# Kernel tuning notes

Measured on AMD Instinct MI355X. Metric: run time of the kernel, lower is better.

## Reference

```python
import jax, jax.numpy as jnp
import numpy as np

SPARSITY = 0.5  # cur_sparsity set during training; 0.0 default would make masking a no-op
WEIGHT_BETA = 1.0
MASK_ALPHA1 = 1.0
MASK_ALPHA2 = 1.0


def binarize(mask_scores, sparsity):
    # SparseBinarizer.forward: prune (set to 0) the `num_prune` smallest scores globally.
    num_prune = int(mask_scores.size * sparsity)  # static: sparsity is a Python float
    flat = mask_scores.reshape(-1)
    prune_idx = jnp.argsort(flat)[:num_prune]
    mask = jnp.ones_like(flat).at[prune_idx].set(0.0)
    return mask.reshape(mask_scores.shape)


def setup_inputs() -> dict:
    key = jax.random.key(0)
    ks = jax.random.split(key, 9)
    out_f, in_f, r = 4096, 4096, 8
    tokens = 8192  # batch 4 * seq 2048
    return {
        "x": jax.random.normal(ks[0], (tokens, in_f), dtype=jnp.float32),
        "weight": jax.random.normal(ks[1], (out_f, in_f), dtype=jnp.float32) * 0.02,
        "bias": jax.random.normal(ks[2], (out_f,), dtype=jnp.float32) * 0.02,
        "weight_U": jax.random.normal(ks[3], (out_f, r), dtype=jnp.float32),
        "weight_V": jnp.zeros((r, in_f), dtype=jnp.float32),
        "mask_scores_A": jax.random.normal(ks[4], (out_f, r), dtype=jnp.float32),
        "mask_scores_B": jnp.zeros((r, in_f), dtype=jnp.float32),
        "mask_scores_R": jnp.zeros((out_f,), dtype=jnp.float32),
        "mask_scores_C": jnp.zeros((in_f,), dtype=jnp.float32),
    }


def reference(x, weight, bias, weight_U, weight_V, mask_scores_A, mask_scores_B,
              mask_scores_R, mask_scores_C):
    # weight = W + beta * U @ V   (low-rank weight reconstruction)
    w = weight + WEIGHT_BETA * (weight_U @ weight_V)
    # mask_scores = |w| + a1 * A @ B + a2 * (R[:,None] + C[None,:])
    mask_scores = (jnp.abs(w)
                   + MASK_ALPHA1 * (mask_scores_A @ mask_scores_B)
                   + MASK_ALPHA2 * (mask_scores_R[:, None] + mask_scores_C[None, :]))
    mask = binarize(mask_scores, SPARSITY)
    masked_weight = mask * w  # [out_f, in_f]
    # nn.Linear: x @ W^T + b
    return x @ masked_weight.T + bias
```

## Files before the change

kernel.cpp:

```cpp
#include <hip/hip_runtime.h>
#include <stdint.h>

#define TOKENS 8192
#define OUT_F  4096
#define IN_F   4096
#define RNK    8
#define RPB    4
#define KPRUNE 8388608u
#define CAP3   16384u

typedef unsigned short u16;
typedef float  f32x4  __attribute__((ext_vector_type(4)));
typedef short  bf16x8 __attribute__((ext_vector_type(8)));
typedef unsigned short u16x8 __attribute__((ext_vector_type(8)));

#define XB_OFF    0ull
#define WB_OFF    67108864ull
#define KEYS_OFF  100663296ull
#define CTL_OFF   167772160ull
#define H1_OFF    0
#define H2_OFF    16384
#define SEL_OFF   32768
#define CNT3_OFF  32800
#define LIST3_OFF 32804
#define CTL_ZERO_U32 8201

__device__ __forceinline__ u16 f2bf(float f) {
    uint32_t u = __float_as_uint(f);
    u += 0x7fffu + ((u >> 16) & 1u);
    return (u16)(u >> 16);
}

__device__ __forceinline__ uint32_t fkey(float s) {
    uint32_t u = __float_as_uint(s);
    return (u & 0x80000000u) ? ~u : (u | 0x80000000u);
}

__global__ void convx_kernel(const float* __restrict__ x, u16* __restrict__ xB,
                             uint32_t* __restrict__ ctl)
{
    const int t = threadIdx.x;
    if (blockIdx.x < 34) {
        const int i = blockIdx.x * 256 + t;
        if (i < CTL_ZERO_U32) ctl[i] = 0u;
    }
    const size_t idx = (size_t)blockIdx.x * 256 + t;
    const float4* xv = (const float4*)x;
    float4 a = xv[idx*2];
    float4 b = xv[idx*2 + 1];
    u16x8 o;
    o[0]=f2bf(a.x); o[1]=f2bf(a.y); o[2]=f2bf(a.z); o[3]=f2bf(a.w);
    o[4]=f2bf(b.x); o[5]=f2bf(b.y); o[6]=f2bf(b.z); o[7]=f2bf(b.w);
    *((u16x8*)xB + idx) = o;
}

__global__ void prep_kernel(const float* __restrict__ W, const float* __restrict__ U,
                            const float* __restrict__ V, const float* __restrict__ A,
                            const float* __restrict__ B, const float* __restrict__ R,
                            const float* __restrict__ C, u16* __restrict__ wB,
                            uint32_t* __restrict__ keys, uint32_t* __restrict__ hist1)
{
    __shared__ uint32_t lh[4096];
    const int o0 = blockIdx.x * RPB, t = threadIdx.x;
    for (int b = t; b < 4096; b += 256) lh[b] = 0u;
    float uu[RPB][RNK], aa[RPB][RNK], ro[RPB];
#pragma unroll
    for (int r0 = 0; r0 < RPB; ++r0) {
#pragma unroll
        for (int r = 0; r < RNK; ++r) {
            uu[r0][r] = U[(o0+r0)*RNK + r];
            aa[r0][r] = A[(o0+r0)*RNK + r];
        }
        ro[r0] = R[o0 + r0];
    }
    __syncthreads();
    for (int j = 0; j < IN_F/256; ++j) {
        const int i = j*256 + t;
        float vv[RNK], bb[RNK];
#pragma unroll
        for (int r = 0; r < RNK; ++r) { vv[r] = V[r*IN_F + i]; bb[r] = B[r*IN_F + i]; }
        const float ci = C[i];
#pragma unroll
        for (int r0 = 0; r0 < RPB; ++r0) {
            float wv = W[(size_t)(o0+r0)*IN_F + i];
#pragma unroll
            for (int r = 0; r < RNK; ++r) wv = fmaf(uu[r0][r], vv[r], wv);
            float s = fabsf(wv);
#pragma unroll
            for (int r = 0; r < RNK; ++r) s = fmaf(aa[r0][r], bb[r], s);
            s += ro[r0] + ci;
            const uint32_t key = fkey(s);
            keys[(size_t)(o0+r0)*IN_F + i] = key;
            wB[(size_t)(o0+r0)*IN_F + i]   = f2bf(wv);
            atomicAdd(&lh[key >> 20], 1u);
        }
    }
    __syncthreads();
    for (int b = t; b < 4096; b += 256) { uint32_t c = lh[b]; if (c) atomicAdd(&hist1[b], c); }
}

__global__ void select_kernel(const uint32_t* __restrict__ hist, uint32_t* sel, int mode)
{
    __shared__ uint32_t lh[4096];
    __shared__ uint32_t part[256];
    __shared__ uint32_t sseg[2];
    const int t = threadIdx.x;
    const uint32_t c1v = sel[1];
    const uint32_t k = (mode == 0) ? KPRUNE : (KPRUNE - c1v);
    for (int b = t; b < 4096; b += 256) lh[b] = hist[b];
    __syncthreads();
    uint32_t s = 0;
    for (int j = 0; j < 16; ++j) s += lh[t*16 + j];
    part[t] = s;
    __syncthreads();
    uint32_t pre = 0;
    for (int tt = 0; tt < t; ++tt) pre += part[tt];
    if (pre < k && pre + part[t] >= k) { sseg[0] = (uint32_t)t; sseg[1] = pre; }
    __syncthreads();
    const int seg = (int)sseg[0];
    const uint32_t accb = sseg[1];
    if (t < 16) {
        uint32_t pre2 = 0;
        for (int j = 0; j < t; ++j) pre2 += lh[seg*16 + j];
        const uint32_t c = lh[seg*16 + t];
        const uint32_t below = accb + pre2;
        if (below < k && below + c >= k) {
            const uint32_t bin = (uint32_t)(seg*16 + t);
            if (mode == 0) { sel[0] = bin; sel[1] = below; }
            else           { sel[2] = bin; sel[3] = c1v + below; }
        }
    }
}

__global__ void hist2_kernel(const uint32_t* __restrict__ keys, const uint32_t* __restrict__ sel,
                             uint32_t* __restrict__ hist2)
{
    __shared__ uint32_t lh[4096];
    const int o = blockIdx.x, t = threadIdx.x;
    const uint32_t b1 = sel[0];
    for (int b = t; b < 4096; b += 256) lh[b] = 0u;
    __syncthreads();
    const uint32_t* kp = keys + (size_t)o*IN_F + t*16;
#pragma unroll
    for (int q = 0; q < 4; ++q) {
        uint4 kv = *(const uint4*)(kp + q*4);
        if ((kv.x >> 20) == b1) atomicAdd(&lh[(kv.x >> 8) & 0xFFFu], 1u);
        if ((kv.y >> 20) == b1) atomicAdd(&lh[(kv.y >> 8) & 0xFFFu], 1u);
        if ((kv.z >> 20) == b1) atomicAdd(&lh[(kv.z >> 8) & 0xFFFu], 1u);
        if ((kv.w >> 20) == b1) atomicAdd(&lh[(kv.w >> 8) & 0xFFFu], 1u);
    }
    __syncthreads();
    for (int b = t; b < 4096; b += 256) { uint32_t c = lh[b]; if (c) atomicAdd(&hist2[b], c); }
}

__global__ void apply_kernel(const uint32_t* __restrict__ keys, const uint32_t* __restrict__ sel,
                             u16* __restrict__ wB, uint32_t* __restrict__ cnt3,
                             uint32_t* __restrict__ list3)
{
    const uint32_t pfx = (sel[0] << 12) | sel[2];
    const size_t base = ((size_t)blockIdx.x * 256 + threadIdx.x) * 16;
    uint32_t kv[16];
#pragma unroll
    for (int q = 0; q < 4; ++q) *(uint4*)(kv + q*4) = *(const uint4*)(keys + base + q*4);
    uint4 wraw[2];
    wraw[0] = *(const uint4*)(wB + base);
    wraw[1] = *(const uint4*)(wB + base + 8);
    u16* wv = (u16*)wraw;
#pragma unroll
    for (int e = 0; e < 16; ++e) {
        const uint32_t hi = kv[e] >> 8;
        if (hi < pfx) wv[e] = 0u;
        else if (hi == pfx) {
            uint32_t s = atomicAdd(cnt3, 1u);
            if (s < CAP3) list3[s] = ((uint32_t)(base + e) << 8) | (kv[e] & 0xFFu);
        }
    }
    *(uint4*)(wB + base)     = wraw[0];
    *(uint4*)(wB + base + 8) = wraw[1];
}

__global__ void selfix_kernel(const uint32_t* __restrict__ sel, const uint32_t* __restrict__ cnt3,
                              const uint32_t* __restrict__ list3, u16* __restrict__ wB)
{
    __shared__ uint32_t lst[CAP3];
    __shared__ uint32_t hist[256];
    __shared__ uint32_t sv[2];
    const int t = threadIdx.x;
    uint32_t n = *cnt3; if (n > CAP3) n = CAP3;
    hist[t] = 0u;
    __syncthreads();
    for (uint32_t i = t; i < n; i += 256) {
        const uint32_t e = list3[i];
        lst[i] = e;
        atomicAdd(&hist[e & 0xFFu], 1u);
    }
    __syncthreads();
    const uint32_t k3 = KPRUNE - sel[3];
    uint32_t pre = 0;
    for (int b = 0; b < t; ++b) pre += hist[b];
    if (pre < k3 && pre + hist[t] >= k3) {
        sv[0] = (uint32_t)t;
        sv[1] = k3 - pre;
    }
    __syncthreads();
    const uint32_t b3 = sv[0], p = sv[1];
    for (uint32_t i = t; i < n; i += 256) {
        const uint32_t e = lst[i];
        const uint32_t lo = e & 0xFFu;
        if (lo < b3) { wB[e >> 8] = 0u; continue; }
        if (lo != b3) continue;
        uint32_t rank = 0;
        for (uint32_t j = 0; j < n; ++j) {
            const uint32_t f = lst[j];
            rank += ((f & 0xFFu) == b3 && f < e) ? 1u : 0u;
        }
        if (rank < p) wB[e >> 8] = 0u;
    }
}

#define A0H0   0
#define A0H1_0 16384
#define A0H1_1 32768
#define B0S    49152
#define A1H0   81920
#define A1H1_0 98304
#define A1H1_1 114688
#define B1S    131072

__device__ __forceinline__ void gl_lds16(const char* src, char* dst) {
    __builtin_amdgcn_global_load_lds((const __attribute__((address_space(1))) void*)src,
                                     (__attribute__((address_space(3))) void*)dst, 16, 0, 0);
}

__global__ __launch_bounds__(512, 2) void gemm256_kernel(const u16* __restrict__ xB,
                                                         const u16* __restrict__ wB,
                                                         const float* __restrict__ bias,
                                                         float* __restrict__ out)
{
    __shared__ char ldsc[163840];
    const int t    = threadIdx.x;
    const int lane = t & 63;
    const int wid  = t >> 6;
    const int wm   = wid >> 2;
    const int wn   = wid & 3;
    const int bid  = blockIdx.x;
    const int bn   = bid & 15;
    const int bm   = bid >> 4;

    const int l15 = lane & 15;
    const int kb  = (lane >> 4) << 4;
    const int sw  = (lane & 7) << 4;
    const int bAo = (16*wm + l15) * 128 + kb;
    const int bB  = (64*wn + l15) * 128 + kb;

    const int scol = ((t & 7) * 16) ^ (((t >> 3) & 7) << 4);
    const char* pA = (const char*)xB + ((size_t)(bm*256 + (t >> 3))) * (IN_F*2) + scol;
    const char* pB = (const char*)wB + ((size_t)(bn*256 + (t >> 3))) * (IN_F*2) + scol;
    const int tb16 = t * 16;

#define STAGEH(pG, slot, h, tile) do {                                        \
    const char* _s = (pG) + (size_t)(tile)*128 + (size_t)(h)*(128*IN_F*2);    \
    char* _d = ldsc + (slot) + tb16;                                          \
    gl_lds16(_s, _d);                                                         \
    gl_lds16(_s + (size_t)(64*IN_F*2), _d + 8192);                            \
} while (0)

    f32x4  acc[8][4] = {};
    bf16x8 b[4][2];
    bf16x8 a[2][2];

#define LOADB(reg) do {                                                       \
    _Pragma("unroll") for (int ni = 0; ni < 4; ++ni)                          \
    _Pragma("unroll") for (int kk = 0; kk < 2; ++kk)                          \
        b[ni][kk] = *(const bf16x8*)(ldsc + (reg) +                           \
                      ((bB + ni*2048 + kk*64) ^ sw));                         \
} while (0)

#define LOADA(slot, q, mo) do {                                               \
    _Pragma("unroll") for (int mm = 0; mm < 2; ++mm)                          \
    _Pragma("unroll") for (int kk = 0; kk < 2; ++kk)                          \
        a[mm][kk] = *(const bf16x8*)(ldsc + (slot) +                          \
                      (((2*(q)+mm-(mo))*4096 + bAo + kk*64) ^ sw));           \
} while (0)

#define MFMAQ(q) do {                                                         \
    _Pragma("unroll") for (int mm = 0; mm < 2; ++mm)                          \
    _Pragma("unroll") for (int ni = 0; ni < 4; ++ni)                          \
    _Pragma("unroll") for (int kk = 0; kk < 2; ++kk)                          \
        acc[2*(q)+mm][ni] = __builtin_amdgcn_mfma_f32_16x16x32_bf16(          \
            a[mm][kk], b[ni][kk], acc[2*(q)+mm][ni], 0, 0, 0);                \
} while (0)

#define PH_TAIL(q)                                                            \
    __builtin_amdgcn_s_barrier();                                             \
    asm volatile("s_waitcnt lgkmcnt(0)" ::: "memory");                        \
    __builtin_amdgcn_s_setprio(1);                                            \
    MFMAQ(q);                                                                 \
    __builtin_amdgcn_s_setprio(0);                                            \
    __builtin_amdgcn_s_barrier();

    STAGEH(pA, A0H1_0, 1, 0);
    STAGEH(pB, B0S,         0, 0);
    STAGEH(pB, B0S + 16384, 1, 0);
    STAGEH(pA, A0H0, 0, 0);
    STAGEH(pA, A1H1_0, 1, 1);
    STAGEH(pB, B1S,         0, 1);
    STAGEH(pB, B1S + 16384, 1, 1);
    STAGEH(pA, A1H0, 0, 1);
    asm volatile("s_waitcnt vmcnt(8)" ::: "memory");
    __builtin_amdgcn_s_barrier();

#pragma unroll 1
    for (int j = 0; j < IN_F/64/2; ++j) {
        const int se = (2*j + 2) & 63;
        const int so = (2*j + 3) & 63;
        const int pc = j & 1;
        const int a0h1c = pc ? A0H1_1 : A0H1_0;
        const int a0h1n = pc ? A0H1_0 : A0H1_1;
        const int a1h1c = pc ? A1H1_1 : A1H1_0;
        const int a1h1n = pc ? A1H1_0 : A1H1_1;

        LOADB(B0S); LOADA(A0H0, 0, 0);
        STAGEH(pA, a0h1n, 1, se);
        asm volatile("s_waitcnt lgkmcnt(8)" ::: "memory");
        PH_TAIL(0)
        LOADA(A0H0, 1, 0);
        STAGEH(pB, B0S, 0, se);
        PH_TAIL(1)
        LOADA(a0h1c, 2, 4);
        STAGEH(pB, B0S + 16384, 1, se);
        PH_TAIL(2)
        LOADA(a0h1c, 3, 4);
        STAGEH(pA, A0H0, 0, se);
        asm volatile("s_waitcnt vmcnt(8)" ::: "memory");
        PH_TAIL(3)

        LOADB(B1S); LOADA(A1H0, 0, 0);
        STAGEH(pA, a1h1n, 1, so);
        asm volatile("s_waitcnt lgkmcnt(8)" ::: "memory");
        PH_TAIL(0)
        LOADA(A1H0, 1, 0);
        STAGEH(pB, B1S, 0, so);
        PH_TAIL(1)
        LOADA(a1h1c, 2, 4);
        STAGEH(pB, B1S + 16384, 1, so);
        PH_TAIL(2)
        LOADA(a1h1c, 3, 4);
        STAGEH(pA, A1H0, 0, so);
        asm volatile("s_waitcnt vmcnt(8)" ::: "memory");
        PH_TAIL(3)
    }

    const int orow0 = bm*256 + 16*wm + ((lane >> 4) << 2);
    const int ocol0 = bn*256 + 64*wn + l15;
#pragma unroll
    for (int ni = 0; ni < 4; ++ni) {
        const int col = ocol0 + ni*16;
        const float bv = bias[col];
#pragma unroll
        for (int m = 0; m < 8; ++m) {
            const int r0 = orow0 + 32*m;
            f32x4 v = acc[m][ni];
#pragma unroll
            for (int q = 0; q < 4; ++q)
                out[(size_t)(r0 + q)*OUT_F + col] = v[q] + bv;
        }
    }
#undef STAGEH
#undef LOADB
#undef LOADA
#undef MFMAQ
#undef PH_TAIL
}

extern "C" void kernel_launch(void* const* d_in, const int* in_sizes, int n_in,
                              void* d_out, int out_size, void* d_ws, size_t ws_size,
                              hipStream_t stream)
{
    const float* x    = (const float*)d_in[0];
    const float* W    = (const float*)d_in[1];
    const float* bias = (const float*)d_in[2];
    const float* U    = (const float*)d_in[3];
    const float* V    = (const float*)d_in[4];
    const float* A    = (const float*)d_in[5];
    const float* B    = (const float*)d_in[6];
    const float* R    = (const float*)d_in[7];
    const float* C    = (const float*)d_in[8];
    float* out = (float*)d_out;

    char* ws = (char*)d_ws;
    u16*      xB    = (u16*)(ws + XB_OFF);
    u16*      wB    = (u16*)(ws + WB_OFF);
    uint32_t* keys  = (uint32_t*)(ws + KEYS_OFF);
    uint32_t* ctl   = (uint32_t*)(ws + CTL_OFF);
    uint32_t* h1    = (uint32_t*)((char*)ctl + H1_OFF);
    uint32_t* h2    = (uint32_t*)((char*)ctl + H2_OFF);
    uint32_t* sel   = (uint32_t*)((char*)ctl + SEL_OFF);
    uint32_t* cnt3  = (uint32_t*)((char*)ctl + CNT3_OFF);
    uint32_t* list3 = (uint32_t*)((char*)ctl + LIST3_OFF);

    convx_kernel<<<TOKENS*IN_F/8/256, 256, 0, stream>>>(x, xB, ctl);
    prep_kernel<<<OUT_F/RPB, 256, 0, stream>>>(W, U, V, A, B, R, C, wB, keys, h1);
    select_kernel<<<1, 256, 0, stream>>>(h1, sel, 0);
    hist2_kernel<<<OUT_F, 256, 0, stream>>>(keys, sel, h2);
    select_kernel<<<1, 256, 0, stream>>>(h2, sel, 1);
    apply_kernel<<<OUT_F, 256, 0, stream>>>(keys, sel, wB, cnt3, list3);
    selfix_kernel<<<1, 256, 0, stream>>>(sel, cnt3, list3, wB);
    gemm256_kernel<<<(TOKENS/256)*(OUT_F/256), 512, 0, stream>>>(xB, wB, bias, out);
}
```

Before: 423.8 us.

## Vectorize prep kernel with two rows per block; peel GEMM tail to overlap stores

The prep kernel now processes two output rows per block with float4 loads and vector stores of keys and bf16 weights, doubling the grid size. The GEMM main loop is shortened by one iteration and the last K-step is peeled, so the final iteration issues no redundant wrapped-around prefetch. Output stores are interleaved with the last MFMA quarters so they overlap compute. This removes wasted global loads at the tail and reduces epilogue latency, at the cost of more code and register pressure.

```diff
diff --git a/kernel.cpp b/kernel.cpp
--- a/kernel.cpp
+++ b/kernel.cpp
@@ -5,13 +5,13 @@
 #define OUT_F  4096
 #define IN_F   4096
 #define RNK    8
-#define RPB    4
 #define KPRUNE 8388608u
 #define CAP3   16384u
 
 typedef unsigned short u16;
 typedef float  f32x4  __attribute__((ext_vector_type(4)));
 typedef short  bf16x8 __attribute__((ext_vector_type(8)));
+typedef unsigned short u16x4 __attribute__((ext_vector_type(4)));
 typedef unsigned short u16x8 __attribute__((ext_vector_type(8)));
 
 #define XB_OFF    0ull
@@ -61,39 +61,58 @@
                             uint32_t* __restrict__ keys, uint32_t* __restrict__ hist1)
 {
     __shared__ uint32_t lh[4096];
-    const int o0 = blockIdx.x * RPB, t = threadIdx.x;
+    const int o0 = blockIdx.x * 2, t = threadIdx.x;
     for (int b = t; b < 4096; b += 256) lh[b] = 0u;
-    float uu[RPB][RNK], aa[RPB][RNK], ro[RPB];
-#pragma unroll
-    for (int r0 = 0; r0 < RPB; ++r0) {
+    float uu0[RNK], uu1[RNK], aa0[RNK], aa1[RNK];
+#pragma unroll
+    for (int r = 0; r < RNK; ++r) {
+        uu0[r] = U[o0*RNK + r];       uu1[r] = U[(o0+1)*RNK + r];
+        aa0[r] = A[o0*RNK + r];       aa1[r] = A[(o0+1)*RNK + r];
+    }
+    const float ro0 = R[o0], ro1 = R[o0 + 1];
+    __syncthreads();
+    for (int j = 0; j < IN_F/1024; ++j) {
+        const int i = j*1024 + t*4;
+        const float4 cc = *(const float4*)&C[i];
+        float4 w0 = *(const float4*)&W[(size_t)o0*IN_F + i];
+        float4 w1 = *(const float4*)&W[(size_t)(o0+1)*IN_F + i];
 #pragma unroll
         for (int r = 0; r < RNK; ++r) {
-            uu[r0][r] = U[(o0+r0)*RNK + r];
-            aa[r0][r] = A[(o0+r0)*RNK + r];
+            const float4 v4 = *(const float4*)&V[r*IN_F + i];
+            const float a0 = uu0[r], a1 = uu1[r];
+            w0.x = fmaf(a0, v4.x, w0.x); w0.y = fmaf(a0, v4.y, w0.y);
+            w0.z = fmaf(a0, v4.z, w0.z); w0.w = fmaf(a0, v4.w, w0.w);
+            w1.x = fmaf(a1, v4.x, w1.x); w1.y = fmaf(a1, v4.y, w1.y);
+            w1.z = fmaf(a1, v4.z, w1.z); w1.w = fmaf(a1, v4.w, w1.w);
         }
-        ro[r0] = R[o0 + r0];
-    }
-    __syncthreads();
-    for (int j = 0; j < IN_F/256; ++j) {
-        const int i = j*256 + t;
-        float vv[RNK], bb[RNK];
-#pragma unroll
-        for (int r = 0; r < RNK; ++r) { vv[r] = V[r*IN_F + i]; bb[r] = B[r*IN_F + i]; }
-        const float ci = C[i];
-#pragma unroll
-        for (int r0 = 0; r0 < RPB; ++r0) {
-            float wv = W[(size_t)(o0+r0)*IN_F + i];
-#pragma unroll
-            for (int r = 0; r < RNK; ++r) wv = fmaf(uu[r0][r], vv[r], wv);
-            float s = fabsf(wv);
-#pragma unroll
-            for (int r = 0; r < RNK; ++r) s = fmaf(aa[r0][r], bb[r], s);
-            s += ro[r0] + ci;
-            const uint32_t key = fkey(s);
-            keys[(size_t)(o0+r0)*IN_F + i] = key;
-            wB[(size_t)(o0+r0)*IN_F + i]   = f2bf(wv);
-            atomicAdd(&lh[key >> 20], 1u);
+        float4 s0, s1;
+        s0.x = fabsf(w0.x); s0.y = fabsf(w0.y); s0.z = fabsf(w0.z); s0.w = fabsf(w0.w);
+        s1.x = fabsf(w1.x); s1.y = fabsf(w1.y); s1.z = fabsf(w1.z); s1.w = fabsf(w1.w);
+#pragma unroll
+        for (int r = 0; r < RNK; ++r) {
+            const float4 b4 = *(const float4*)&B[r*IN_F + i];
+            const float a0 = aa0[r], a1 = aa1[r];
+            s0.x = fmaf(a0, b4.x, s0.x); s0.y = fmaf(a0, b4.y, s0.y);
+            s0.z = fmaf(a0, b4.z, s0.z); s0.w = fmaf(a0, b4.w, s0.w);
+            s1.x = fmaf(a1, b4.x, s1.x); s1.y = fmaf(a1, b4.y, s1.y);
+            s1.z = fmaf(a1, b4.z, s1.z); s1.w = fmaf(a1, b4.w, s1.w);
         }
+        s0.x += ro0 + cc.x; s0.y += ro0 + cc.y; s0.z += ro0 + cc.z; s0.w += ro0 + cc.w;
+        s1.x += ro1 + cc.x; s1.y += ro1 + cc.y; s1.z += ro1 + cc.z; s1.w += ro1 + cc.w;
+        uint4 k0, k1;
+        k0.x = fkey(s0.x); k0.y = fkey(s0.y); k0.z = fkey(s0.z); k0.w = fkey(s0.w);
+        k1.x = fkey(s1.x); k1.y = fkey(s1.y); k1.z = fkey(s1.z); k1.w = fkey(s1.w);
+        *(uint4*)&keys[(size_t)o0*IN_F + i]     = k0;
+        *(uint4*)&keys[(size_t)(o0+1)*IN_F + i] = k1;
+        u16x4 b0, b1;
+        b0[0]=f2bf(w0.x); b0[1]=f2bf(w0.y); b0[2]=f2bf(w0.z); b0[3]=f2bf(w0.w);
+        b1[0]=f2bf(w1.x); b1[1]=f2bf(w1.y); b1[2]=f2bf(w1.z); b1[3]=f2bf(w1.w);
+        *(u16x4*)&wB[(size_t)o0*IN_F + i]     = b0;
+        *(u16x4*)&wB[(size_t)(o0+1)*IN_F + i] = b1;
+        atomicAdd(&lh[k0.x >> 20], 1u); atomicAdd(&lh[k0.y >> 20], 1u);
+        atomicAdd(&lh[k0.z >> 20], 1u); atomicAdd(&lh[k0.w >> 20], 1u);
+        atomicAdd(&lh[k1.x >> 20], 1u); atomicAdd(&lh[k1.y >> 20], 1u);
+        atomicAdd(&lh[k1.z >> 20], 1u); atomicAdd(&lh[k1.w >> 20], 1u);
     }
     __syncthreads();
     for (int b = t; b < 4096; b += 256) { uint32_t c = lh[b]; if (c) atomicAdd(&hist1[b], c); }
@@ -299,6 +318,27 @@
     __builtin_amdgcn_s_setprio(0);                                            \
     __builtin_amdgcn_s_barrier();
 
+#define STQ(q) do {                                                           \
+    _Pragma("unroll") for (int mm = 0; mm < 2; ++mm) {                        \
+        const int r0 = orow0 + 32*(2*(q)+mm);                                 \
+        _Pragma("unroll") for (int ni = 0; ni < 4; ++ni) {                    \
+            f32x4 v = acc[2*(q)+mm][ni];                                      \
+            const int col = ocol0 + ni*16;                                    \
+            _Pragma("unroll") for (int e = 0; e < 4; ++e)                     \
+                out[(size_t)(r0 + e)*OUT_F + col] = v[e] + bv[ni];            \
+        }                                                                     \
+    }                                                                         \
+} while (0)
+
+#define PH_TAIL_ST(q)                                                         \
+    __builtin_amdgcn_s_barrier();                                             \
+    asm volatile("s_waitcnt lgkmcnt(0)" ::: "memory");                        \
+    __builtin_amdgcn_s_setprio(1);                                            \
+    MFMAQ(q);                                                                 \
+    __builtin_amdgcn_s_setprio(0);                                            \
+    STQ(q);                                                                   \
+    __builtin_amdgcn_s_barrier();
+
     STAGEH(pA, A0H1_0, 1, 0);
     STAGEH(pB, B0S,         0, 0);
     STAGEH(pB, B0S + 16384, 1, 0);
@@ -311,9 +351,9 @@
     __builtin_amdgcn_s_barrier();
 
 #pragma unroll 1
-    for (int j = 0; j < IN_F/64/2; ++j) {
-        const int se = (2*j + 2) & 63;
-        const int so = (2*j + 3) & 63;
+    for (int j = 0; j < 31; ++j) {
+        const int se = 2*j + 2;
+        const int so = 2*j + 3;
         const int pc = j & 1;
         const int a0h1c = pc ? A0H1_1 : A0H1_0;
         const int a0h1n = pc ? A0H1_0 : A0H1_1;
@@ -353,24 +393,39 @@
 
     const int orow0 = bm*256 + 16*wm + ((lane >> 4) << 2);
     const int ocol0 = bn*256 + 64*wn + l15;
-#pragma unroll
-    for (int ni = 0; ni < 4; ++ni) {
-        const int col = ocol0 + ni*16;
-        const float bv = bias[col];
-#pragma unroll
-        for (int m = 0; m < 8; ++m) {
-            const int r0 = orow0 + 32*m;
-            f32x4 v = acc[m][ni];
-#pragma unroll
-            for (int q = 0; q < 4; ++q)
-                out[(size_t)(r0 + q)*OUT_F + col] = v[q] + bv;
-        }
-    }
+    float bv[4];
+#pragma unroll
+    for (int ni = 0; ni < 4; ++ni) bv[ni] = bias[ocol0 + ni*16];
+
+    LOADB(B0S); LOADA(A0H0, 0, 0);
+    asm volatile("s_waitcnt lgkmcnt(8)" ::: "memory");
+    PH_TAIL(0)
+    LOADA(A0H0, 1, 0);
+    PH_TAIL(1)
+    LOADA(A0H1_1, 2, 4);
+    PH_TAIL(2)
+    LOADA(A0H1_1, 3, 4);
+    PH_TAIL(3)
+
+    asm volatile("s_waitcnt vmcnt(0)" ::: "memory");
+    __builtin_amdgcn_s_barrier();
+    LOADB(B1S); LOADA(A1H0, 0, 0);
+    asm volatile("s_waitcnt lgkmcnt(8)" ::: "memory");
+    PH_TAIL_ST(0)
+    LOADA(A1H0, 1, 0);
+    PH_TAIL_ST(1)
+    LOADA(A1H1_1, 2, 4);
+    PH_TAIL_ST(2)
+    LOADA(A1H1_1, 3, 4);
+    PH_TAIL_ST(3)
+
 #undef STAGEH
 #undef LOADB
 #undef LOADA
 #undef MFMAQ
 #undef PH_TAIL
+#undef PH_TAIL_ST
+#undef STQ
 }
 
 extern "C" void kernel_launch(void* const* d_in, const int* in_sizes, int n_in,
@@ -400,7 +455,7 @@
     uint32_t* list3 = (uint32_t*)((char*)ctl + LIST3_OFF);
 
     convx_kernel<<<TOKENS*IN_F/8/256, 256, 0, stream>>>(x, xB, ctl);
-    prep_kernel<<<OUT_F/RPB, 256, 0, stream>>>(W, U, V, A, B, R, C, wB, keys, h1);
+    prep_kernel<<<OUT_F/2, 256, 0, stream>>>(W, U, V, A, B, R, C, wB, keys, h1);
     select_kernel<<<1, 256, 0, stream>>>(h1, sel, 0);
     hist2_kernel<<<OUT_F, 256, 0, stream>>>(keys, sel, h2);
     select_kernel<<<1, 256, 0, stream>>>(h2, sel, 1);
```

New measurement: 401.6 us. -5.2%, faster.
